# Optimization experiments

Measured on AMD Instinct MI355X. Metric: run time of the kernel, lower is better.

Reference implementation:

```python
import jax, jax.numpy as jnp
import numpy as np

B, N, C, D = 64, 1024, 128, 64

def setup_inputs() -> dict:
    key = jax.random.key(0)
    ks = jax.random.split(key, 7)
    # kaiming_normal_ on weights (fan_in = C), default zero-ish biases kept as Linear default uniform; use small uniform
    std = float(np.sqrt(2.0 / C))
    bb = float(1.0 / np.sqrt(C))
    return {
        "x": jax.random.normal(ks[0], (B, N, C), jnp.float32),
        "Wq": jax.random.normal(ks[1], (C, D), jnp.float32) * std,
        "bq": jax.random.uniform(ks[2], (D,), jnp.float32, -bb, bb),
        "Wk": jax.random.normal(ks[3], (C, D), jnp.float32) * std,
        "bk": jax.random.uniform(ks[4], (D,), jnp.float32, -bb, bb),
        "Wv": jax.random.normal(ks[5], (C, D), jnp.float32) * std,
        "bv": jax.random.uniform(ks[6], (D,), jnp.float32, -bb, bb),
    }

def reference(x, Wq, bq, Wk, bk, Wv, bv):
    q = jax.nn.relu(jnp.einsum('bnc,cd->bnd', x, Wq) + bq)  # [B,N,D]
    k = jax.nn.relu(jnp.einsum('bnc,cd->bnd', x, Wk) + bk)
    v = jax.nn.relu(jnp.einsum('bnc,cd->bnd', x, Wv) + bv)
    scores = jnp.einsum('bnd,bmd->bnm', q, k) / jnp.sqrt(jnp.asarray(D, q.dtype))
    attn = jax.nn.softmax(scores, axis=-1)
    out = jnp.einsum('bnm,bmd->bnd', attn, v)
    return out + q
```

## Files before the change

kernel.cpp:

```cpp
#include <hip/hip_runtime.h>
#include <hip/hip_bf16.h>


#define Bsz 64
#define Nsz 1024
#define Csz 128
#define Dsz 64

typedef __attribute__((ext_vector_type(8))) short short8;
typedef __attribute__((ext_vector_type(4))) float f32x4;

__device__ __forceinline__ unsigned short f2bf(float f) {
    union { float f; unsigned u; } v; v.f = f;
    unsigned r = v.u + 0x7FFF + ((v.u >> 16) & 1);
    return (unsigned short)(r >> 16);
}
__device__ __forceinline__ float bf2f(unsigned short h) {
    union { unsigned u; float f; } v; v.u = ((unsigned)h) << 16;
    return v.f;
}
__device__ __forceinline__ unsigned pack_bf16rn(float lo, float hi) {
    unsigned ulo = __float_as_uint(lo) + 0x8000u;
    unsigned uhi = __float_as_uint(hi) + 0x8000u;
    return __builtin_amdgcn_perm(uhi, ulo, 0x07060302u);
}

#define SCq (0.125f * 1.44269504f)
#define INV_SC (1.0f / (0.125f * 1.44269504f))

__global__ __launch_bounds__(256) void wprep_kernel(
    const float* __restrict__ Wq, const float* __restrict__ Wk,
    const float* __restrict__ Wv, unsigned short* __restrict__ wfrag)
{
    int t = blockIdx.x * 256 + threadIdx.x;
    int lane = t & 63, ksi = (t >> 6) & 3, dt = t >> 8;
    int l16 = lane & 15, quad = lane >> 4;
    int d = dt * 16 + l16;
    int c0 = ksi * 32 + quad * 8;
    short8 h8, l8, k8, v8;
    #pragma unroll
    for (int j = 0; j < 8; j++) {
        float w = Wq[(c0 + j) * Dsz + d];
        unsigned short h = f2bf(w);
        h8[j] = (short)h;
        l8[j] = (short)f2bf(w - bf2f(h));
        k8[j] = (short)f2bf(Wk[(c0 + j) * Dsz + d]);
        v8[j] = (short)f2bf(Wv[(c0 + j) * Dsz + d]);
    }
    int idx = (dt * 4 + ksi) * 64 + lane;
    ((short8*)wfrag)[0 * 1024 + idx] = h8;
    ((short8*)wfrag)[1 * 1024 + idx] = l8;
    ((short8*)wfrag)[2 * 1024 + idx] = k8;
    ((short8*)wfrag)[3 * 1024 + idx] = v8;
}

__global__ __launch_bounds__(256, 2) void fused_kernel(
    const float* __restrict__ x, const unsigned short* __restrict__ wfrag,
    const float* __restrict__ bq, const float* __restrict__ bk,
    const float* __restrict__ bv, float* __restrict__ out)
{
    __shared__ short Xs[8192];
    __shared__ short KVb[2][4096];
    __shared__ short Qs[128][72];
    __shared__ short Pl[4][32][72];

    const int t    = threadIdx.x;
    const int lane = t & 63;
    const int l16  = lane & 15;
    const int quad = lane >> 4;
    const int wave = t >> 6;
    const int dt   = wave;
    const int b    = blockIdx.x & 63;
    const int qh   = blockIdx.x >> 6;
    const int d    = dt * 16 + l16;

    short8 wqh[4], wql[4], wkf[4], wvf[4];
    #pragma unroll
    for (int ksi = 0; ksi < 4; ksi++) {
        int idx = (dt * 4 + ksi) * 64 + lane;
        wqh[ksi] = ((const short8*)wfrag)[0 * 1024 + idx];
        wql[ksi] = ((const short8*)wfrag)[1 * 1024 + idx];
        wkf[ksi] = ((const short8*)wfrag)[2 * 1024 + idx];
        wvf[ksi] = ((const short8*)wfrag)[3 * 1024 + idx];
    }
    const float bqd = bq[d], bkd = bk[d], bvd = bv[d];

    #pragma unroll 1
    for (int h64 = 0; h64 < 2; h64++) {
        const long rowbase = (long)b * Nsz + qh * 128 + h64 * 64;
        {
            const int row = t & 63;
            const float* xrow = x + (rowbase + row) * Csz;
            short* xl = &KVb[0][0];
            #pragma unroll
            for (int p = 0; p < 4; p++) {
                int cb = (t >> 6) + p * 4;
                float4 a  = *(const float4*)(xrow + cb * 8);
                float4 b2 = *(const float4*)(xrow + cb * 8 + 4);
                float f[8] = {a.x, a.y, a.z, a.w, b2.x, b2.y, b2.z, b2.w};
                short8 hi, lo;
                #pragma unroll
                for (int i = 0; i < 8; i++) {
                    unsigned short h = f2bf(f[i]);
                    hi[i] = (short)h;
                    lo[i] = (short)f2bf(f[i] - bf2f(h));
                }
                int unit = ((row >> 4) * 4 + (cb >> 2)) * 64 + ((row & 15) | ((cb & 3) << 4));
                *(short8*)&Xs[unit * 8] = hi;
                *(short8*)&xl[unit * 8] = lo;
            }
        }
        __syncthreads();
        f32x4 aqc[4];
        #pragma unroll
        for (int i = 0; i < 4; i++) aqc[i] = (f32x4){0.f, 0.f, 0.f, 0.f};
        #pragma unroll
        for (int ksi = 0; ksi < 4; ksi++) {
            #pragma unroll
            for (int rt = 0; rt < 4; rt++) {
                short8 ah = *(const short8*)&Xs[((rt * 4 + ksi) * 64 + lane) * 8];
                short8 al = *(const short8*)&KVb[0][((rt * 4 + ksi) * 64 + lane) * 8];
                aqc[rt] = __builtin_amdgcn_mfma_f32_16x16x32_bf16(ah, wqh[ksi], aqc[rt], 0, 0, 0);
                aqc[rt] = __builtin_amdgcn_mfma_f32_16x16x32_bf16(al, wqh[ksi], aqc[rt], 0, 0, 0);
                aqc[rt] = __builtin_amdgcn_mfma_f32_16x16x32_bf16(ah, wql[ksi], aqc[rt], 0, 0, 0);
            }
        }
        #pragma unroll
        for (int rt = 0; rt < 4; rt++)
            #pragma unroll
            for (int r = 0; r < 4; r++) {
                float q = fmaxf(aqc[rt][r] + bqd, 0.f);
                Qs[h64 * 64 + rt * 16 + quad * 4 + r][d] = f2bf(q * SCq);
            }
        __syncthreads();
    }

    short8 aq[2][2];
    #pragma unroll
    for (int s = 0; s < 2; s++) {
        aq[s][0] = *(const short8*)&Qs[wave * 32 + s * 16 + l16][quad * 8];
        aq[s][1] = *(const short8*)&Qs[wave * 32 + s * 16 + l16][32 + quad * 8];
    }

    f32x4 O[2][4];
    float lsum[2][4];
    #pragma unroll
    for (int s = 0; s < 2; s++)
        #pragma unroll
        for (int i = 0; i < 4; i++) { O[s][i] = (f32x4){0.f,0.f,0.f,0.f}; lsum[s][i] = 0.f; }

    const int half  = dt >> 1;
    const int quadk = ((dt & 1) << 1) | (l16 >> 3);
    const int jk    = l16 & 7;
    const int ckk   = quad >> 1;
    const int quadp = (quad & 1) * 2;

    #pragma unroll 1
    for (int kt = 0; kt < 16; kt++) {
        {
            const long rowbase = (long)b * Nsz + kt * 64;
            const int row = t & 63;
            const float* xrow = x + (rowbase + row) * Csz;
            #pragma unroll
            for (int p = 0; p < 4; p++) {
                int cb = (t >> 6) + p * 4;
                float4 a  = *(const float4*)(xrow + cb * 8);
                float4 b2 = *(const float4*)(xrow + cb * 8 + 4);
                float f[8] = {a.x, a.y, a.z, a.w, b2.x, b2.y, b2.z, b2.w};
                short8 hi;
                #pragma unroll
                for (int i = 0; i < 8; i++) hi[i] = (short)f2bf(f[i]);
                int unit = ((row >> 4) * 4 + (cb >> 2)) * 64 + ((row & 15) | ((cb & 3) << 4));
                *(short8*)&Xs[unit * 8] = hi;
            }
        }
        __syncthreads();

        f32x4 ak[4], av[4];
        #pragma unroll
        for (int i = 0; i < 4; i++) {
            ak[i] = (f32x4){0.f, 0.f, 0.f, 0.f};
            av[i] = (f32x4){0.f, 0.f, 0.f, 0.f};
        }
        #pragma unroll
        for (int ksi = 0; ksi < 4; ksi++) {
            #pragma unroll
            for (int rt = 0; rt < 4; rt++) {
                short8 ah = *(const short8*)&Xs[((rt * 4 + ksi) * 64 + lane) * 8];
                ak[rt] = __builtin_amdgcn_mfma_f32_16x16x32_bf16(ah, wkf[ksi], ak[rt], 0, 0, 0);
                av[rt] = __builtin_amdgcn_mfma_f32_16x16x32_bf16(ah, wvf[ksi], av[rt], 0, 0, 0);
            }
        }
        float vv[4][4];
        #pragma unroll
        for (int rt = 0; rt < 4; rt++) {
            #pragma unroll
            for (int r = 0; r < 4; r++) {
                float kv = fmaxf(ak[rt][r] + bkd, 0.f);
                vv[r][rt] = fmaxf(av[rt][r] + bvd, 0.f);
                KVb[0][(rt * 2 + half) * 512 + (quadk * 16 + quad * 4 + r) * 8 + jk] = f2bf(kv);
            }
        }
        uint4 o0 = make_uint4(pack_bf16rn(vv[0][0], vv[0][1]), pack_bf16rn(vv[0][2], vv[0][3]),
                              pack_bf16rn(vv[1][0], vv[1][1]), pack_bf16rn(vv[1][2], vv[1][3]));
        uint4 o1 = make_uint4(pack_bf16rn(vv[2][0], vv[2][1]), pack_bf16rn(vv[2][2], vv[2][3]),
                              pack_bf16rn(vv[3][0], vv[3][1]), pack_bf16rn(vv[3][2], vv[3][3]));
        *(uint4*)&KVb[1][(dt * 2 + ckk) * 512 + (quadp * 16 + l16) * 8]      = o0;
        *(uint4*)&KVb[1][(dt * 2 + ckk) * 512 + (quadp * 16 + 16 + l16) * 8] = o1;
        __syncthreads();

        short8 kf[4][2];
        #pragma unroll
        for (int kb = 0; kb < 4; kb++) {
            kf[kb][0] = *(const short8*)&KVb[0][(kb * 2 + 0) * 512 + lane * 8];
            kf[kb][1] = *(const short8*)&KVb[0][(kb * 2 + 1) * 512 + lane * 8];
        }
        f32x4 sc[2][4];
        #pragma unroll
        for (int s = 0; s < 2; s++) {
            #pragma unroll
            for (int kb = 0; kb < 4; kb++) {
                f32x4 z = (f32x4){0.f, 0.f, 0.f, 0.f};
                z = __builtin_amdgcn_mfma_f32_16x16x32_bf16(aq[s][0], kf[kb][0], z, 0, 0, 0);
                z = __builtin_amdgcn_mfma_f32_16x16x32_bf16(aq[s][1], kf[kb][1], z, 0, 0, 0);
                sc[s][kb] = z;
            }
        }
        short8 bvf[2][4];
        #pragma unroll
        for (int cb = 0; cb < 4; cb++) {
            bvf[0][cb] = *(const short8*)&KVb[1][(cb * 2 + 0) * 512 + lane * 8];
            bvf[1][cb] = *(const short8*)&KVb[1][(cb * 2 + 1) * 512 + lane * 8];
        }
        #pragma unroll
        for (int s = 0; s < 2; s++) {
            #pragma unroll
            for (int r = 0; r < 4; r++) {
                float p0 = __builtin_amdgcn_exp2f(sc[s][0][r]);
                float p1 = __builtin_amdgcn_exp2f(sc[s][1][r]);
                float p2 = __builtin_amdgcn_exp2f(sc[s][2][r]);
                float p3 = __builtin_amdgcn_exp2f(sc[s][3][r]);
                lsum[s][r] += (p0 + p1) + (p2 + p3);
                *(uint2*)&Pl[wave][s * 16 + quad * 4 + r][l16 * 4] =
                    make_uint2(pack_bf16rn(p0, p1), pack_bf16rn(p2, p3));
            }
        }
        #pragma unroll
        for (int ck = 0; ck < 2; ck++) {
            #pragma unroll
            for (int s = 0; s < 2; s++) {
                short8 ap = *(const short8*)&Pl[wave][s * 16 + l16][ck * 32 + quad * 8];
                #pragma unroll
                for (int cb = 0; cb < 4; cb++) {
                    O[s][cb] = __builtin_amdgcn_mfma_f32_16x16x32_bf16(ap, bvf[ck][cb], O[s][cb], 0, 0, 0);
                }
            }
        }
        __syncthreads();
    }

    #pragma unroll
    for (int s = 0; s < 2; s++)
        #pragma unroll
        for (int r = 0; r < 4; r++)
            #pragma unroll
            for (int off = 1; off < 16; off <<= 1)
                lsum[s][r] += __shfl_xor(lsum[s][r], off);

    #pragma unroll
    for (int s = 0; s < 2; s++) {
        #pragma unroll
        for (int r = 0; r < 4; r++) {
            float rl = 1.0f / lsum[s][r];
            int lrow = wave * 32 + s * 16 + quad * 4 + r;
            long nrow = (long)b * Nsz + qh * 128 + lrow;
            #pragma unroll
            for (int cb = 0; cb < 4; cb++) {
                int d2 = cb * 16 + l16;
                float qv = bf2f((unsigned short)Qs[lrow][d2]) * INV_SC;
                out[nrow * Dsz + d2] = O[s][cb][r] * rl + qv;
            }
        }
    }
}

extern "C" void kernel_launch(void* const* d_in, const int* in_sizes, int n_in,
                              void* d_out, int out_size, void* d_ws, size_t ws_size,
                              hipStream_t stream) {
    const float* x  = (const float*)d_in[0];
    const float* Wq = (const float*)d_in[1];
    const float* bq = (const float*)d_in[2];
    const float* Wk = (const float*)d_in[3];
    const float* bk = (const float*)d_in[4];
    const float* Wv = (const float*)d_in[5];
    const float* bv = (const float*)d_in[6];
    float* out = (float*)d_out;

    unsigned short* wfrag = (unsigned short*)d_ws;

    wprep_kernel<<<dim3(4), dim3(256), 0, stream>>>(Wq, Wk, Wv, wfrag);
    fused_kernel<<<dim3(512), dim3(256), 0, stream>>>(
        x, wfrag, bq, bk, bv, out);
}
```

Before: 149.4 us.

## Halve query rows per block, inline weight prep, and prefetch next X tile

```diff
diff --git a/kernel.cpp b/kernel.cpp
--- a/kernel.cpp
+++ b/kernel.cpp
@@ -28,41 +28,17 @@
 #define SCq (0.125f * 1.44269504f)
 #define INV_SC (1.0f / (0.125f * 1.44269504f))
 
-__global__ __launch_bounds__(256) void wprep_kernel(
-    const float* __restrict__ Wq, const float* __restrict__ Wk,
-    const float* __restrict__ Wv, unsigned short* __restrict__ wfrag)
-{
-    int t = blockIdx.x * 256 + threadIdx.x;
-    int lane = t & 63, ksi = (t >> 6) & 3, dt = t >> 8;
-    int l16 = lane & 15, quad = lane >> 4;
-    int d = dt * 16 + l16;
-    int c0 = ksi * 32 + quad * 8;
-    short8 h8, l8, k8, v8;
-    #pragma unroll
-    for (int j = 0; j < 8; j++) {
-        float w = Wq[(c0 + j) * Dsz + d];
-        unsigned short h = f2bf(w);
-        h8[j] = (short)h;
-        l8[j] = (short)f2bf(w - bf2f(h));
-        k8[j] = (short)f2bf(Wk[(c0 + j) * Dsz + d]);
-        v8[j] = (short)f2bf(Wv[(c0 + j) * Dsz + d]);
-    }
-    int idx = (dt * 4 + ksi) * 64 + lane;
-    ((short8*)wfrag)[0 * 1024 + idx] = h8;
-    ((short8*)wfrag)[1 * 1024 + idx] = l8;
-    ((short8*)wfrag)[2 * 1024 + idx] = k8;
-    ((short8*)wfrag)[3 * 1024 + idx] = v8;
-}
-
-__global__ __launch_bounds__(256, 2) void fused_kernel(
-    const float* __restrict__ x, const unsigned short* __restrict__ wfrag,
-    const float* __restrict__ bq, const float* __restrict__ bk,
-    const float* __restrict__ bv, float* __restrict__ out)
+__global__ __launch_bounds__(256, 3) void fused_kernel(
+    const float* __restrict__ x,
+    const float* __restrict__ Wq, const float* __restrict__ bq,
+    const float* __restrict__ Wk, const float* __restrict__ bk,
+    const float* __restrict__ Wv, const float* __restrict__ bv,
+    float* __restrict__ out)
 {
     __shared__ short Xs[8192];
     __shared__ short KVb[2][4096];
-    __shared__ short Qs[128][72];
-    __shared__ short Pl[4][32][72];
+    __shared__ short Qs[64][72];
+    __shared__ short Pl[4][16][72];
 
     const int t    = threadIdx.x;
     const int lane = t & 63;
@@ -74,20 +50,32 @@
     const int qh   = blockIdx.x >> 6;
     const int d    = dt * 16 + l16;
 
-    short8 wqh[4], wql[4], wkf[4], wvf[4];
+    short8 wqh[4], wkf[4], wvf[4];
     #pragma unroll
     for (int ksi = 0; ksi < 4; ksi++) {
-        int idx = (dt * 4 + ksi) * 64 + lane;
-        wqh[ksi] = ((const short8*)wfrag)[0 * 1024 + idx];
-        wql[ksi] = ((const short8*)wfrag)[1 * 1024 + idx];
-        wkf[ksi] = ((const short8*)wfrag)[2 * 1024 + idx];
-        wvf[ksi] = ((const short8*)wfrag)[3 * 1024 + idx];
+        int c0 = ksi * 32 + quad * 8;
+        #pragma unroll
+        for (int j = 0; j < 8; j++) {
+            wqh[ksi][j] = (short)f2bf(Wq[(c0 + j) * Dsz + d]);
+            wkf[ksi][j] = (short)f2bf(Wk[(c0 + j) * Dsz + d]);
+            wvf[ksi][j] = (short)f2bf(Wv[(c0 + j) * Dsz + d]);
+        }
     }
     const float bqd = bq[d], bkd = bk[d], bvd = bv[d];
 
-    #pragma unroll 1
-    for (int h64 = 0; h64 < 2; h64++) {
-        const long rowbase = (long)b * Nsz + qh * 128 + h64 * 64;
+    {
+        short8 wql[4];
+        #pragma unroll
+        for (int ksi = 0; ksi < 4; ksi++) {
+            int c0 = ksi * 32 + quad * 8;
+            #pragma unroll
+            for (int j = 0; j < 8; j++) {
+                float w = Wq[(c0 + j) * Dsz + d];
+                unsigned short h = f2bf(w);
+                wql[ksi][j] = (short)f2bf(w - bf2f(h));
+            }
+        }
+        const long rowbase = (long)b * Nsz + qh * 64;
         {
             const int row = t & 63;
             const float* xrow = x + (rowbase + row) * Csz;
@@ -130,24 +118,19 @@
             #pragma unroll
             for (int r = 0; r < 4; r++) {
                 float q = fmaxf(aqc[rt][r] + bqd, 0.f);
-                Qs[h64 * 64 + rt * 16 + quad * 4 + r][d] = f2bf(q * SCq);
-            }
-        __syncthreads();
-    }
-
-    short8 aq[2][2];
-    #pragma unroll
-    for (int s = 0; s < 2; s++) {
-        aq[s][0] = *(const short8*)&Qs[wave * 32 + s * 16 + l16][quad * 8];
-        aq[s][1] = *(const short8*)&Qs[wave * 32 + s * 16 + l16][32 + quad * 8];
-    }
-
-    f32x4 O[2][4];
-    float lsum[2][4];
-    #pragma unroll
-    for (int s = 0; s < 2; s++)
-        #pragma unroll
-        for (int i = 0; i < 4; i++) { O[s][i] = (f32x4){0.f,0.f,0.f,0.f}; lsum[s][i] = 0.f; }
+                Qs[rt * 16 + quad * 4 + r][d] = f2bf(q * SCq);
+            }
+        __syncthreads();
+    }
+
+    short8 aq[2];
+    aq[0] = *(const short8*)&Qs[wave * 16 + l16][quad * 8];
+    aq[1] = *(const short8*)&Qs[wave * 16 + l16][32 + quad * 8];
+
+    f32x4 O[4];
+    float lsum[4];
+    #pragma unroll
+    for (int i = 0; i < 4; i++) { O[i] = (f32x4){0.f,0.f,0.f,0.f}; lsum[i] = 0.f; }
 
     const int half  = dt >> 1;
     const int quadk = ((dt & 1) << 1) | (l16 >> 3);
@@ -155,26 +138,38 @@
     const int ckk   = quad >> 1;
     const int quadp = (quad & 1) * 2;
 
+    float4 xa[4], xb[4];
+    auto load_x = [&](int kt2) {
+        const float* xrow = x + ((long)b * Nsz + kt2 * 64 + (t & 63)) * Csz;
+        #pragma unroll
+        for (int p = 0; p < 4; p++) {
+            int cb = (t >> 6) + p * 4;
+            xa[p] = *(const float4*)(xrow + cb * 8);
+            xb[p] = *(const float4*)(xrow + cb * 8 + 4);
+        }
+    };
+    auto write_xs = [&]() {
+        const int row = t & 63;
+        #pragma unroll
+        for (int p = 0; p < 4; p++) {
+            int cb = (t >> 6) + p * 4;
+            float f[8] = {xa[p].x, xa[p].y, xa[p].z, xa[p].w,
+                          xb[p].x, xb[p].y, xb[p].z, xb[p].w};
+            short8 hi;
+            #pragma unroll
+            for (int i = 0; i < 8; i++) hi[i] = (short)f2bf(f[i]);
+            int unit = ((row >> 4) * 4 + (cb >> 2)) * 64 + ((row & 15) | ((cb & 3) << 4));
+            *(short8*)&Xs[unit * 8] = hi;
+        }
+    };
+
+    load_x(0);
+    write_xs();
+    __syncthreads();
+
     #pragma unroll 1
     for (int kt = 0; kt < 16; kt++) {
-        {
-            const long rowbase = (long)b * Nsz + kt * 64;
-            const int row = t & 63;
-            const float* xrow = x + (rowbase + row) * Csz;
-            #pragma unroll
-            for (int p = 0; p < 4; p++) {
-                int cb = (t >> 6) + p * 4;
-                float4 a  = *(const float4*)(xrow + cb * 8);
-                float4 b2 = *(const float4*)(xrow + cb * 8 + 4);
-                float f[8] = {a.x, a.y, a.z, a.w, b2.x, b2.y, b2.z, b2.w};
-                short8 hi;
-                #pragma unroll
-                for (int i = 0; i < 8; i++) hi[i] = (short)f2bf(f[i]);
-                int unit = ((row >> 4) * 4 + (cb >> 2)) * 64 + ((row & 15) | ((cb & 3) << 4));
-                *(short8*)&Xs[unit * 8] = hi;
-            }
-        }
-        __syncthreads();
+        if (kt < 15) load_x(kt + 1);
 
         f32x4 ak[4], av[4];
         #pragma unroll
@@ -207,7 +202,10 @@
                               pack_bf16rn(vv[3][0], vv[3][1]), pack_bf16rn(vv[3][2], vv[3][3]));
         *(uint4*)&KVb[1][(dt * 2 + ckk) * 512 + (quadp * 16 + l16) * 8]      = o0;
         *(uint4*)&KVb[1][(dt * 2 + ckk) * 512 + (quadp * 16 + 16 + l16) * 8] = o1;
-        __syncthreads();
+
+        __syncthreads();
+
+        if (kt < 15) write_xs();
 
         short8 kf[4][2];
         #pragma unroll
@@ -215,16 +213,13 @@
             kf[kb][0] = *(const short8*)&KVb[0][(kb * 2 + 0) * 512 + lane * 8];
             kf[kb][1] = *(const short8*)&KVb[0][(kb * 2 + 1) * 512 + lane * 8];
         }
-        f32x4 sc[2][4];
-        #pragma unroll
-        for (int s = 0; s < 2; s++) {
-            #pragma unroll
-            for (int kb = 0; kb < 4; kb++) {
-                f32x4 z = (f32x4){0.f, 0.f, 0.f, 0.f};
-                z = __builtin_amdgcn_mfma_f32_16x16x32_bf16(aq[s][0], kf[kb][0], z, 0, 0, 0);
-                z = __builtin_amdgcn_mfma_f32_16x16x32_bf16(aq[s][1], kf[kb][1], z, 0, 0, 0);
-                sc[s][kb] = z;
-            }
+        f32x4 sc[4];
+        #pragma unroll
+        for (int kb = 0; kb < 4; kb++) {
+            f32x4 z = (f32x4){0.f, 0.f, 0.f, 0.f};
+            z = __builtin_amdgcn_mfma_f32_16x16x32_bf16(aq[0], kf[kb][0], z, 0, 0, 0);
+            z = __builtin_amdgcn_mfma_f32_16x16x32_bf16(aq[1], kf[kb][1], z, 0, 0, 0);
+            sc[kb] = z;
         }
         short8 bvf[2][4];
         #pragma unroll
@@ -233,53 +228,43 @@
             bvf[1][cb] = *(const short8*)&KVb[1][(cb * 2 + 1) * 512 + lane * 8];
         }
         #pragma unroll
-        for (int s = 0; s < 2; s++) {
-            #pragma unroll
-            for (int r = 0; r < 4; r++) {
-                float p0 = __builtin_amdgcn_exp2f(sc[s][0][r]);
-                float p1 = __builtin_amdgcn_exp2f(sc[s][1][r]);
-                float p2 = __builtin_amdgcn_exp2f(sc[s][2][r]);
-                float p3 = __builtin_amdgcn_exp2f(sc[s][3][r]);
-                lsum[s][r] += (p0 + p1) + (p2 + p3);
-                *(uint2*)&Pl[wave][s * 16 + quad * 4 + r][l16 * 4] =
-                    make_uint2(pack_bf16rn(p0, p1), pack_bf16rn(p2, p3));
-            }
+        for (int r = 0; r < 4; r++) {
+            float p0 = __builtin_amdgcn_exp2f(sc[0][r]);
+            float p1 = __builtin_amdgcn_exp2f(sc[1][r]);
+            float p2 = __builtin_amdgcn_exp2f(sc[2][r]);
+            float p3 = __builtin_amdgcn_exp2f(sc[3][r]);
+            lsum[r] += (p0 + p1) + (p2 + p3);
+            *(uint2*)&Pl[wave][quad * 4 + r][l16 * 4] =
+                make_uint2(pack_bf16rn(p0, p1), pack_bf16rn(p2, p3));
         }
         #pragma unroll
         for (int ck = 0; ck < 2; ck++) {
-            #pragma unroll
-            for (int s = 0; s < 2; s++) {
-                short8 ap = *(const short8*)&Pl[wave][s * 16 + l16][ck * 32 + quad * 8];
-                #pragma unroll
-                for (int cb = 0; cb < 4; cb++) {
-                    O[s][cb] = __builtin_amdgcn_mfma_f32_16x16x32_bf16(ap, bvf[ck][cb], O[s][cb], 0, 0, 0);
-                }
-            }
-        }
-        __syncthreads();
-    }
-
-    #pragma unroll
-    for (int s = 0; s < 2; s++)
-        #pragma unroll
-        for (int r = 0; r < 4; r++)
-            #pragma unroll
-            for (int off = 1; off < 16; off <<= 1)
-                lsum[s][r] += __shfl_xor(lsum[s][r], off);
-
-    #pragma unroll
-    for (int s = 0; s < 2; s++) {
-        #pragma unroll
-        for (int r = 0; r < 4; r++) {
-            float rl = 1.0f / lsum[s][r];
-            int lrow = wave * 32 + s * 16 + quad * 4 + r;
-            long nrow = (long)b * Nsz + qh * 128 + lrow;
+            short8 ap = *(const short8*)&Pl[wave][l16][ck * 32 + quad * 8];
             #pragma unroll
             for (int cb = 0; cb < 4; cb++) {
-                int d2 = cb * 16 + l16;
-                float qv = bf2f((unsigned short)Qs[lrow][d2]) * INV_SC;
-                out[nrow * Dsz + d2] = O[s][cb][r] * rl + qv;
-            }
+                O[cb] = __builtin_amdgcn_mfma_f32_16x16x32_bf16(ap, bvf[ck][cb], O[cb], 0, 0, 0);
+            }
+        }
+
+        __syncthreads();
+    }
+
+    #pragma unroll
+    for (int r = 0; r < 4; r++)
+        #pragma unroll
+        for (int off = 1; off < 16; off <<= 1)
+            lsum[r] += __shfl_xor(lsum[r], off);
+
+    #pragma unroll
+    for (int r = 0; r < 4; r++) {
+        float rl = 1.0f / lsum[r];
+        int lrow = wave * 16 + quad * 4 + r;
+        long nrow = (long)b * Nsz + qh * 64 + lrow;
+        #pragma unroll
+        for (int cb = 0; cb < 4; cb++) {
+            int d2 = cb * 16 + l16;
+            float qv = bf2f((unsigned short)Qs[lrow][d2]) * INV_SC;
+            out[nrow * Dsz + d2] = O[cb][r] * rl + qv;
         }
     }
 }
@@ -296,9 +281,6 @@
     const float* bv = (const float*)d_in[6];
     float* out = (float*)d_out;
 
-    unsigned short* wfrag = (unsigned short*)d_ws;
-
-    wprep_kernel<<<dim3(4), dim3(256), 0, stream>>>(Wq, Wk, Wv, wfrag);
-    fused_kernel<<<dim3(512), dim3(256), 0, stream>>>(
-        x, wfrag, bq, bk, bv, out);
-}
+    fused_kernel<<<dim3(1024), dim3(256), 0, stream>>>(
+        x, Wq, bq, Wk, bk, Wv, bv, out);
+}
```

Measured after the change: 170.5 us. 1.14x slower.
